# Kernel optimization log

Measured on AMD Instinct MI355X. Metric: run time of the kernel, lower is better.

The kernel has to match this reference:

```python
import jax, jax.numpy as jnp
import numpy as np

B, T, E, H = 4, 2048, 1024, 16
D = E // H

def setup_inputs() -> dict:
    key = jax.random.key(0)
    ks = jax.random.split(key, 8)
    s = 0.02
    return {
        "q": jax.random.normal(ks[0], (B, T, E), dtype=jnp.float32),
        "k": jax.random.normal(ks[1], (B, T, E), dtype=jnp.float32),
        "v": jax.random.normal(ks[2], (B, T, E), dtype=jnp.float32),
        "Wq": jax.random.normal(ks[3], (E, E), dtype=jnp.float32) * s,
        "Wk": jax.random.normal(ks[4], (E, E), dtype=jnp.float32) * s,
        "Wv": jax.random.normal(ks[5], (E, E), dtype=jnp.float32) * s,
        "Wp": jax.random.normal(ks[6], (E, E), dtype=jnp.float32) * s,
        "bp": jnp.zeros((E,), dtype=jnp.float32),
    }

def reference(q, k, v, Wq, Wk, Wv, Wp, bp):
    # Linear projections (torch Linear: x @ W.T). NOTE: original code computes
    # key from the already-projected query (k = self.key(q)); external k is unused.
    qp = q @ Wq.T                      # [B,T,E]
    kp = qp @ Wk.T                     # [B,T,E]  <- faithful quirk
    vp = v @ Wv.T                      # [B,T,E]
    qh = qp.reshape(B, T, H, D).transpose(0, 2, 1, 3)  # [B,H,T,D]
    kh = kp.reshape(B, T, H, D).transpose(0, 2, 1, 3)
    vh = vp.reshape(B, T, H, D).transpose(0, 2, 1, 3)
    # Faithful quirk: att = scores / D**(-1/2) == scores * sqrt(D)
    scale = jnp.float32(D) ** 0.5
    att = jnp.einsum('bhtd,bhsd->bhts', qh, kh) * scale  # [B,H,T,T]
    causal = jnp.tril(jnp.ones((T, T), dtype=bool))
    att = jnp.where(causal, att, -jnp.inf)
    att = jax.nn.softmax(att, axis=-1)
    y = jnp.einsum('bhts,bhsd->bhtd', att, vh)           # [B,H,T,D]
    y = y.transpose(0, 2, 1, 3).reshape(B, T, E)
    return y @ Wp.T + bp
```

## Files before the change

### kernel.cpp

```cpp
#include <hip/hip_runtime.h>


typedef unsigned short u16;
typedef unsigned int   u32;
typedef __attribute__((ext_vector_type(8))) __bf16 bf16x8;
typedef __attribute__((ext_vector_type(8))) u16    u16x8;
typedef __attribute__((ext_vector_type(4))) u16    u16x4;
typedef __attribute__((ext_vector_type(4))) float  f32x4;
typedef __attribute__((ext_vector_type(4))) int    i32x4;

#define DEV static __device__ __forceinline__

DEV u16 f2bf(float x){ union{float f;u32 u;}v; v.f=x; u32 r=v.u+0x7fffu+((v.u>>16)&1u); return (u16)(r>>16); }
DEV float bf2f(u16 b){ union{u32 u;float f;}v; v.u=((u32)b)<<16; return v.f; }
DEV f32x4 zero4(){ f32x4 z={0.f,0.f,0.f,0.f}; return z; }
DEV f32x4 mfma16(bf16x8 a, bf16x8 b, f32x4 c){ return __builtin_amdgcn_mfma_f32_16x16x32_bf16(a,b,c,0,0,0); }
DEV void gld16(const u16* g, u16* l){
  __builtin_amdgcn_global_load_lds((const __attribute__((address_space(1))) u32*)g,
                                   (__attribute__((address_space(3))) u32*)l, 16, 0, 0);
}

constexpr int B_=4, T_=2048, E_=1024;
constexpr int M_=B_*T_;

__global__ __launch_bounds__(256) void cvt_w(const float* __restrict__ Wq, const float* __restrict__ Wk,
                                             const float* __restrict__ Wv,
                                             u16* wqh,u16* wql,u16* wkh,u16* wkl,u16* wvb)
{
  const int j=blockIdx.y;
  const float* s = (j==0)?Wq : (j==1)?Wk : Wv;
  size_t i = ((size_t)blockIdx.x*256 + threadIdx.x)*4;
  f32x4 v = *reinterpret_cast<const f32x4*>(s+i);
  u16x4 h,l;
#pragma unroll
  for(int t=0;t<4;t++){ u16 hh=f2bf(v[t]); h[t]=hh; l[t]=f2bf(v[t]-bf2f(hh)); }
  if(j==0){ *reinterpret_cast<u16x4*>(wqh+i)=h; *reinterpret_cast<u16x4*>(wql+i)=l; }
  else if(j==1){ *reinterpret_cast<u16x4*>(wkh+i)=h; *reinterpret_cast<u16x4*>(wkl+i)=l; }
  else { *reinterpret_cast<u16x4*>(wvb+i)=h; }
}

__global__ __launch_bounds__(256) void cvt_a(const float* __restrict__ q, const float* __restrict__ v,
                                             u16* qsh,u16* qsl,u16* vb)
{
  const int j=blockIdx.y;
  size_t i = ((size_t)blockIdx.x*256 + threadIdx.x)*4;
  const float* s = (j==0)?q:v;
  f32x4 x = *reinterpret_cast<const f32x4*>(s+i);
  u16x4 h,l;
#pragma unroll
  for(int t=0;t<4;t++){ u16 hh=f2bf(x[t]); h[t]=hh; l[t]=f2bf(x[t]-bf2f(hh)); }
  if(j==0){ *reinterpret_cast<u16x4*>(qsh+i)=h; *reinterpret_cast<u16x4*>(qsl+i)=l; }
  else { *reinterpret_cast<u16x4*>(vb+i)=h; }
}

template<int ASPLIT,int WSPLIT,int WF32,int OMODE>
__global__ __launch_bounds__(256)
void gemm(const u16* __restrict__ Ah, const u16* __restrict__ Al,
          const u16* __restrict__ Wh, const u16* __restrict__ Wl,
          const float* __restrict__ Wf, const float* __restrict__ bias,
          u16* __restrict__ Ohi, u16* __restrict__ Olo, float* __restrict__ Of)
{
  constexpr int WPIT = WF32 ? 40 : 32;
  __shared__ u16 sAh[128*32];
  __shared__ u16 sAl[ASPLIT?128*32:8];
  __shared__ u16 sBh[128*WPIT];
  __shared__ u16 sBl[WSPLIT?128*WPIT:8];

  const int tid=threadIdx.x, wave=tid>>6, lane=tid&63;
  const int quad=lane>>4, l16=lane&15;
  const int wm=(wave>>1)*64, wn=(wave&1)*64;
  const int n0=blockIdx.x*128, m0=blockIdx.y*128;

  f32x4 acc[4][4];
#pragma unroll
  for(int i=0;i<4;i++)
#pragma unroll
    for(int j=0;j<4;j++) acc[i][j]=zero4();

  for(int k0=0;k0<E_;k0+=32){
#pragma unroll
    for(int it=0;it<2;it++){
      const int chunk=it*256+tid;
      const size_t goff=(size_t)(m0+(chunk>>2))*E_ + k0 + (chunk&3)*8;
      u16* ldst=&sAh[(it*256+wave*64)*8];
      gld16(Ah+goff, ldst);
      if(ASPLIT) gld16(Al+goff, &sAl[(it*256+wave*64)*8]);
    }
    if(!WF32){
#pragma unroll
      for(int it=0;it<2;it++){
        const int chunk=it*256+tid;
        const size_t goff=(size_t)(n0+(chunk>>2))*E_ + k0 + (chunk&3)*8;
        gld16(Wh+goff, &sBh[(it*256+wave*64)*8]);
        if(WSPLIT) gld16(Wl+goff, &sBl[(it*256+wave*64)*8]);
      }
    } else {
#pragma unroll
      for(int it=0;it<4;it++){
        int c=it*256+tid, row=c>>3, col=(c&7)*4;
        f32x4 w=*reinterpret_cast<const f32x4*>(Wf + (size_t)(n0+row)*E_ + k0+col);
        u16x4 h;
#pragma unroll
        for(int t=0;t<4;t++) h[t]=f2bf(w[t]);
        *reinterpret_cast<u16x4*>(&sBh[row*WPIT+col])=h;
      }
    }
    __syncthreads();

    bf16x8 ah[4],bh[4],al[4],bl[4];
#pragma unroll
    for(int i=0;i<4;i++){
      ah[i]=*reinterpret_cast<const bf16x8*>(&sAh[(wm+i*16+l16)*32+quad*8]);
      bh[i]=*reinterpret_cast<const bf16x8*>(&sBh[(wn+i*16+l16)*WPIT+quad*8]);
      if(ASPLIT) al[i]=*reinterpret_cast<const bf16x8*>(&sAl[(wm+i*16+l16)*32+quad*8]);
      if(WSPLIT) bl[i]=*reinterpret_cast<const bf16x8*>(&sBl[(wn+i*16+l16)*WPIT+quad*8]);
    }
#pragma unroll
    for(int i=0;i<4;i++)
#pragma unroll
      for(int j=0;j<4;j++){
        acc[i][j]=mfma16(ah[i],bh[j],acc[i][j]);
        if(WSPLIT) acc[i][j]=mfma16(ah[i],bl[j],acc[i][j]);
        if(ASPLIT) acc[i][j]=mfma16(al[i],bh[j],acc[i][j]);
      }
    __syncthreads();
  }

#pragma unroll
  for(int i=0;i<4;i++)
#pragma unroll
    for(int j=0;j<4;j++){
      const int col=n0+wn+j*16+l16;
#pragma unroll
      for(int r=0;r<4;r++){
        const int row=m0+wm+i*16+quad*4+r;
        const size_t idx=(size_t)row*E_+col;
        float v=acc[i][j][r];
        if(OMODE==2)      Of[idx]=v+bias[col];
        else if(OMODE==1) Ohi[idx]=f2bf(v);
        else { u16 hh=f2bf(v); Ohi[idx]=hh; Olo[idx]=f2bf(v-bf2f(hh)); }
      }
    }
}

__global__ __launch_bounds__(256)
void attn(const u16* __restrict__ qph, const u16* __restrict__ qpl,
          const u16* __restrict__ kph, const u16* __restrict__ kpl,
          const u16* __restrict__ vph, u16* __restrict__ yout)
{
  constexpr int VP=72;
  __shared__ u16 sKh[64*64];
  __shared__ u16 sKl[64*64];
  __shared__ u16 sV [64*VP];

  const int tid=threadIdx.x, wave=tid>>6, lane=tid&63;
  const int quad=lane>>4, l16=lane&15;
  const int qt = (int)(gridDim.x-1-blockIdx.x)>>6;
  const int bh = blockIdx.x&63;
  const int b=bh>>4, h=bh&15;
  const int qr0=qt*128+wave*32;

  bf16x8 qfh[2][2], qfl[2][2];
#pragma unroll
  for(int mt=0;mt<2;mt++)
#pragma unroll
    for(int ksv=0;ksv<2;ksv++){
      size_t off=(size_t)(b*T_+qr0+mt*16+l16)*E_ + h*64 + ksv*32 + quad*8;
      qfh[mt][ksv]=*reinterpret_cast<const bf16x8*>(qph+off);
      qfl[mt][ksv]=*reinterpret_cast<const bf16x8*>(qpl+off);
    }

  float mst[2]={-1e30f,-1e30f}, lst[2]={0.f,0.f};
  f32x4 oacc[2][4];
#pragma unroll
  for(int mt=0;mt<2;mt++)
#pragma unroll
    for(int dt=0;dt<4;dt++) oacc[mt][dt]=zero4();

  const int nkt=2*(qt+1);
  for(int kt=0;kt<nkt;kt++){
    const int s0=kt*64;
    __syncthreads();
#pragma unroll
    for(int it=0;it<2;it++){
      const int chunk=it*256+tid;
      const size_t off=(size_t)(b*T_+s0+(chunk>>3))*E_ + h*64 + (chunk&7)*8;
      gld16(kph+off, &sKh[(it*256+wave*64)*8]);
      gld16(kpl+off, &sKl[(it*256+wave*64)*8]);
    }
#pragma unroll
    for(int it=0;it<2;it++){
      const int c=it*256+tid, s=c&63, dc=(c>>6)*8;
      u16x8 vv=*reinterpret_cast<const u16x8*>(vph + (size_t)(b*T_+s0+s)*E_ + h*64 + dc);
#pragma unroll
      for(int j=0;j<8;j++) sV[(dc+j)*VP+s]=vv[j];
    }
    __syncthreads();

    if(s0<=qr0+31){
      f32x4 sacc[4][2];
#pragma unroll
      for(int st=0;st<4;st++)
#pragma unroll
        for(int mt=0;mt<2;mt++) sacc[st][mt]=zero4();
#pragma unroll
      for(int st=0;st<4;st++)
#pragma unroll
        for(int ksv=0;ksv<2;ksv++){
          bf16x8 kh=*reinterpret_cast<const bf16x8*>(&sKh[(st*16+l16)*64+ksv*32+quad*8]);
          bf16x8 kl=*reinterpret_cast<const bf16x8*>(&sKl[(st*16+l16)*64+ksv*32+quad*8]);
#pragma unroll
          for(int mt=0;mt<2;mt++){
            sacc[st][mt]=mfma16(kh,qfh[mt][ksv],sacc[st][mt]);
            sacc[st][mt]=mfma16(kl,qfh[mt][ksv],sacc[st][mt]);
            sacc[st][mt]=mfma16(kh,qfl[mt][ksv],sacc[st][mt]);
          }
        }
      const bool needmask=(s0+63>qr0);
      u32 pk_[4][2][2];
#pragma unroll
      for(int mt=0;mt<2;mt++){
        const int qrow=qr0+mt*16+l16;
        float mloc=-1e30f;
#pragma unroll
        for(int st=0;st<4;st++)
#pragma unroll
          for(int r=0;r<4;r++){
            float v=sacc[st][mt][r]*8.0f;
            if(needmask && (s0+st*16+quad*4+r>qrow)) v=-1e30f;
            sacc[st][mt][r]=v;
            mloc=fmaxf(mloc,v);
          }
        mloc=fmaxf(mloc,__shfl_xor(mloc,16,64));
        mloc=fmaxf(mloc,__shfl_xor(mloc,32,64));
        const float nm=fmaxf(mst[mt],mloc);
        const float alpha=__expf(mst[mt]-nm);
        mst[mt]=nm;
        float rs=0.f;
#pragma unroll
        for(int st=0;st<4;st++)
#pragma unroll
          for(int r=0;r<4;r++){
            float p=__expf(sacc[st][mt][r]-nm);
            sacc[st][mt][r]=p;
            rs+=p;
          }
        rs+=__shfl_xor(rs,16,64);
        rs+=__shfl_xor(rs,32,64);
        lst[mt]=lst[mt]*alpha+rs;
#pragma unroll
        for(int dt=0;dt<4;dt++) oacc[mt][dt]*=alpha;
#pragma unroll
        for(int st=0;st<4;st++){
          pk_[st][mt][0]=(u32)f2bf(sacc[st][mt][0]) | ((u32)f2bf(sacc[st][mt][1])<<16);
          pk_[st][mt][1]=(u32)f2bf(sacc[st][mt][2]) | ((u32)f2bf(sacc[st][mt][3])<<16);
        }
      }
      const int srcA=(2*(quad&1))*16+l16, srcB=srcA+16;
      const bool hs=(quad>=2);
#pragma unroll
      for(int ksv=0;ksv<2;ksv++){
        bf16x8 b2[2];
#pragma unroll
        for(int mt=0;mt<2;mt++){
          int e0=__shfl((int)pk_[2*ksv  ][mt][0],srcA,64);
          int g0=__shfl((int)pk_[2*ksv+1][mt][0],srcA,64);
          int e1=__shfl((int)pk_[2*ksv  ][mt][1],srcA,64);
          int g1=__shfl((int)pk_[2*ksv+1][mt][1],srcA,64);
          int e2=__shfl((int)pk_[2*ksv  ][mt][0],srcB,64);
          int g2=__shfl((int)pk_[2*ksv+1][mt][0],srcB,64);
          int e3=__shfl((int)pk_[2*ksv  ][mt][1],srcB,64);
          int g3=__shfl((int)pk_[2*ksv+1][mt][1],srcB,64);
          i32x4 bd={ hs?g0:e0, hs?g1:e1, hs?g2:e2, hs?g3:e3 };
          b2[mt]=*reinterpret_cast<bf16x8*>(&bd);
        }
#pragma unroll
        for(int dt=0;dt<4;dt++){
          bf16x8 va=*reinterpret_cast<const bf16x8*>(&sV[(dt*16+l16)*VP+ksv*32+quad*8]);
#pragma unroll
          for(int mt=0;mt<2;mt++)
            oacc[mt][dt]=mfma16(va,b2[mt],oacc[mt][dt]);
        }
      }
    }
  }
#pragma unroll
  for(int mt=0;mt<2;mt++){
    const float inv=1.0f/lst[mt];
    const size_t rb=(size_t)(b*T_+qr0+mt*16+l16)*E_ + h*64;
#pragma unroll
    for(int dt=0;dt<4;dt++){
      u16x4 o4;
#pragma unroll
      for(int r=0;r<4;r++) o4[r]=f2bf(oacc[mt][dt][r]*inv);
      *reinterpret_cast<u16x4*>(yout + rb + dt*16 + quad*4)=o4;
    }
  }
}

extern "C" void kernel_launch(void* const* d_in, const int* in_sizes, int n_in,
                              void* d_out, int out_size, void* d_ws, size_t ws_size,
                              hipStream_t stream)
{
  const float* q =(const float*)d_in[0];
  const float* v =(const float*)d_in[2];
  const float* Wq=(const float*)d_in[3];
  const float* Wk=(const float*)d_in[4];
  const float* Wv=(const float*)d_in[5];
  const float* Wp=(const float*)d_in[6];
  const float* bp=(const float*)d_in[7];
  float* out=(float*)d_out;

  const size_t NE=(size_t)M_*E_;
  u16* ws0=(u16*)d_ws;
  u16* ws1=ws0+NE;
  u16* ws2=ws1+NE;
  u16* ws3=ws2+NE;
  u16* ws4=ws3+NE;
  u16* ws5=ws4+NE;
  const size_t WE=(size_t)E_*E_;
  u16* wqh=(u16*)d_out;
  u16* wql=wqh+WE;
  u16* wkh=wql+WE;
  u16* wkl=wkh+WE;
  u16* wvb=wkl+WE;

  dim3 blk(256);
  cvt_a<<<dim3(NE/1024,2), blk, 0, stream>>>(q, v, ws2, ws3, ws5);
  cvt_w<<<dim3(WE/1024,3), blk, 0, stream>>>(Wq, Wk, Wv, wqh, wql, wkh, wkl, wvb);

  dim3 g(E_/128, M_/128);
  gemm<1,1,0,0><<<g, blk, 0, stream>>>(ws2, ws3, wqh, wql, nullptr, nullptr, ws0, ws1, nullptr);
  gemm<1,1,0,0><<<g, blk, 0, stream>>>(ws0, ws1, wkh, wkl, nullptr, nullptr, ws2, ws3, nullptr);
  gemm<0,0,0,1><<<g, blk, 0, stream>>>(ws5, nullptr, wvb, nullptr, nullptr, nullptr, ws4, nullptr, nullptr);
  attn<<<dim3(16*64), blk, 0, stream>>>(ws0, ws1, ws2, ws3, ws4, ws5);
  gemm<0,0,1,2><<<g, blk, 0, stream>>>(ws5, nullptr, nullptr, nullptr, Wp, bp, nullptr, nullptr, out);
}
```

Measured before the change: 484.7 us.

## Interleave hi/lo bf16 splits, swizzle LDS tiles, widen GEMM K-step, use exp2 softmax

```diff
diff --git a/kernel.cpp b/kernel.cpp
--- a/kernel.cpp
+++ b/kernel.cpp
@@ -19,57 +19,77 @@
   __builtin_amdgcn_global_load_lds((const __attribute__((address_space(1))) u32*)g,
                                    (__attribute__((address_space(3))) u32*)l, 16, 0, 0);
 }
+DEV u32 pkbf(float a, float b){
+  union{float f;u32 u;}x,y; x.f=a; y.f=b;
+  return __builtin_amdgcn_perm(y.u+0x8000u, x.u+0x8000u, 0x07060302u);
+}
 
 constexpr int B_=4, T_=2048, E_=1024;
 constexpr int M_=B_*T_;
-
-__global__ __launch_bounds__(256) void cvt_w(const float* __restrict__ Wq, const float* __restrict__ Wk,
-                                             const float* __restrict__ Wv,
-                                             u16* wqh,u16* wql,u16* wkh,u16* wkl,u16* wvb)
+constexpr float L2E8 = 11.5415603f;
+
+__global__ __launch_bounds__(256)
+void cvt_a(const float* __restrict__ q, const float* __restrict__ v,
+           u16* __restrict__ qi, u16* __restrict__ vb)
 {
   const int j=blockIdx.y;
-  const float* s = (j==0)?Wq : (j==1)?Wk : Wv;
-  size_t i = ((size_t)blockIdx.x*256 + threadIdx.x)*4;
-  f32x4 v = *reinterpret_cast<const f32x4*>(s+i);
-  u16x4 h,l;
-#pragma unroll
-  for(int t=0;t<4;t++){ u16 hh=f2bf(v[t]); h[t]=hh; l[t]=f2bf(v[t]-bf2f(hh)); }
-  if(j==0){ *reinterpret_cast<u16x4*>(wqh+i)=h; *reinterpret_cast<u16x4*>(wql+i)=l; }
-  else if(j==1){ *reinterpret_cast<u16x4*>(wkh+i)=h; *reinterpret_cast<u16x4*>(wkl+i)=l; }
-  else { *reinterpret_cast<u16x4*>(wvb+i)=h; }
-}
-
-__global__ __launch_bounds__(256) void cvt_a(const float* __restrict__ q, const float* __restrict__ v,
-                                             u16* qsh,u16* qsl,u16* vb)
+  const size_t e=((size_t)blockIdx.x*256+threadIdx.x)*8;
+  const float* s=(j==0)?q:v;
+  f32x4 x0=*reinterpret_cast<const f32x4*>(s+e);
+  f32x4 x1=*reinterpret_cast<const f32x4*>(s+e+4);
+  u16x8 h,l;
+#pragma unroll
+  for(int t=0;t<4;t++){
+    u16 hh=f2bf(x0[t]); h[t]=hh; l[t]=f2bf(x0[t]-bf2f(hh));
+    u16 h2=f2bf(x1[t]); h[t+4]=h2; l[t+4]=f2bf(x1[t]-bf2f(h2));
+  }
+  if(j==0){
+    const size_t row=e>>10, k=e&1023;
+    u16* d=qi + row*2048 + (k>>3)*16;
+    *reinterpret_cast<u16x8*>(d)=h;
+    *reinterpret_cast<u16x8*>(d+8)=l;
+  } else {
+    *reinterpret_cast<u16x8*>(vb+e)=h;
+  }
+}
+
+__global__ __launch_bounds__(256)
+void cvt_w(const float* __restrict__ Wq, const float* __restrict__ Wk, const float* __restrict__ Wv,
+           u16* __restrict__ wqi, u16* __restrict__ wki, u16* __restrict__ wvb)
 {
   const int j=blockIdx.y;
-  size_t i = ((size_t)blockIdx.x*256 + threadIdx.x)*4;
-  const float* s = (j==0)?q:v;
-  f32x4 x = *reinterpret_cast<const f32x4*>(s+i);
-  u16x4 h,l;
-#pragma unroll
-  for(int t=0;t<4;t++){ u16 hh=f2bf(x[t]); h[t]=hh; l[t]=f2bf(x[t]-bf2f(hh)); }
-  if(j==0){ *reinterpret_cast<u16x4*>(qsh+i)=h; *reinterpret_cast<u16x4*>(qsl+i)=l; }
-  else { *reinterpret_cast<u16x4*>(vb+i)=h; }
-}
-
-template<int ASPLIT,int WSPLIT,int WF32,int OMODE>
+  const size_t e=((size_t)blockIdx.x*256+threadIdx.x)*8;
+  const float* s=(j==0)?Wq:(j==1)?Wk:Wv;
+  f32x4 x0=*reinterpret_cast<const f32x4*>(s+e);
+  f32x4 x1=*reinterpret_cast<const f32x4*>(s+e+4);
+  u16x8 h,l;
+#pragma unroll
+  for(int t=0;t<4;t++){
+    u16 hh=f2bf(x0[t]); h[t]=hh; l[t]=f2bf(x0[t]-bf2f(hh));
+    u16 h2=f2bf(x1[t]); h[t+4]=h2; l[t+4]=f2bf(x1[t]-bf2f(h2));
+  }
+  if(j==2){ *reinterpret_cast<u16x8*>(wvb+e)=h; return; }
+  u16* base=(j==0)?wqi:wki;
+  const size_t row=e>>10, k=e&1023;
+  u16* d=base + row*2048 + (k>>3)*16;
+  *reinterpret_cast<u16x8*>(d)=h;
+  *reinterpret_cast<u16x8*>(d+8)=l;
+}
+
+template<int SPLIT,int WF32,int OMODE>
 __global__ __launch_bounds__(256)
-void gemm(const u16* __restrict__ Ah, const u16* __restrict__ Al,
-          const u16* __restrict__ Wh, const u16* __restrict__ Wl,
+void gemm(const u16* __restrict__ Ag, const u16* __restrict__ Bg,
           const float* __restrict__ Wf, const float* __restrict__ bias,
-          u16* __restrict__ Ohi, u16* __restrict__ Olo, float* __restrict__ Of)
-{
-  constexpr int WPIT = WF32 ? 40 : 32;
-  __shared__ u16 sAh[128*32];
-  __shared__ u16 sAl[ASPLIT?128*32:8];
-  __shared__ u16 sBh[128*WPIT];
-  __shared__ u16 sBl[WSPLIT?128*WPIT:8];
+          u16* __restrict__ Ob, float* __restrict__ Of)
+{
+  __shared__ u16 sA[128*64];
+  __shared__ u16 sB[WF32 ? 128*68 : 128*64];
 
   const int tid=threadIdx.x, wave=tid>>6, lane=tid&63;
-  const int quad=lane>>4, l16=lane&15;
+  const int quad=lane>>4, l16=lane&15, sw=l16&7;
   const int wm=(wave>>1)*64, wn=(wave&1)*64;
   const int n0=blockIdx.x*128, m0=blockIdx.y*128;
+  constexpr int KSTEP = SPLIT?32:64;
 
   f32x4 acc[4][4];
 #pragma unroll
@@ -77,52 +97,71 @@
 #pragma unroll
     for(int j=0;j<4;j++) acc[i][j]=zero4();
 
-  for(int k0=0;k0<E_;k0+=32){
-#pragma unroll
-    for(int it=0;it<2;it++){
-      const int chunk=it*256+tid;
-      const size_t goff=(size_t)(m0+(chunk>>2))*E_ + k0 + (chunk&3)*8;
-      u16* ldst=&sAh[(it*256+wave*64)*8];
-      gld16(Ah+goff, ldst);
-      if(ASPLIT) gld16(Al+goff, &sAl[(it*256+wave*64)*8]);
+  for(int k0=0;k0<E_;k0+=KSTEP){
+#pragma unroll
+    for(int it=0;it<4;it++){
+      const int c=it*256+tid, row=c>>3, j=(c&7)^(row&7);
+      const u16* ga = SPLIT ? Ag + (size_t)(m0+row)*2048 + (size_t)(k0>>3)*16 + j*8
+                            : Ag + (size_t)(m0+row)*1024 + k0 + j*8;
+      gld16(ga, &sA[(it*256+wave*64)*8]);
     }
     if(!WF32){
 #pragma unroll
-      for(int it=0;it<2;it++){
-        const int chunk=it*256+tid;
-        const size_t goff=(size_t)(n0+(chunk>>2))*E_ + k0 + (chunk&3)*8;
-        gld16(Wh+goff, &sBh[(it*256+wave*64)*8]);
-        if(WSPLIT) gld16(Wl+goff, &sBl[(it*256+wave*64)*8]);
+      for(int it=0;it<4;it++){
+        const int c=it*256+tid, row=c>>3, j=(c&7)^(row&7);
+        const u16* gb = SPLIT ? Bg + (size_t)(n0+row)*2048 + (size_t)(k0>>3)*16 + j*8
+                              : Bg + (size_t)(n0+row)*1024 + k0 + j*8;
+        gld16(gb, &sB[(it*256+wave*64)*8]);
       }
     } else {
 #pragma unroll
-      for(int it=0;it<4;it++){
-        int c=it*256+tid, row=c>>3, col=(c&7)*4;
-        f32x4 w=*reinterpret_cast<const f32x4*>(Wf + (size_t)(n0+row)*E_ + k0+col);
-        u16x4 h;
-#pragma unroll
-        for(int t=0;t<4;t++) h[t]=f2bf(w[t]);
-        *reinterpret_cast<u16x4*>(&sBh[row*WPIT+col])=h;
+      for(int it=0;it<8;it++){
+        const int idx=it*256+tid, row=idx>>4, col=(idx&15)*4;
+        f32x4 w=*reinterpret_cast<const f32x4*>(Wf + (size_t)(n0+row)*1024 + k0+col);
+        u16x4 hh;
+#pragma unroll
+        for(int t=0;t<4;t++) hh[t]=f2bf(w[t]);
+        *reinterpret_cast<u16x4*>(&sB[row*68+col])=hh;
       }
     }
     __syncthreads();
 
-    bf16x8 ah[4],bh[4],al[4],bl[4];
-#pragma unroll
-    for(int i=0;i<4;i++){
-      ah[i]=*reinterpret_cast<const bf16x8*>(&sAh[(wm+i*16+l16)*32+quad*8]);
-      bh[i]=*reinterpret_cast<const bf16x8*>(&sBh[(wn+i*16+l16)*WPIT+quad*8]);
-      if(ASPLIT) al[i]=*reinterpret_cast<const bf16x8*>(&sAl[(wm+i*16+l16)*32+quad*8]);
-      if(WSPLIT) bl[i]=*reinterpret_cast<const bf16x8*>(&sBl[(wn+i*16+l16)*WPIT+quad*8]);
-    }
-#pragma unroll
-    for(int i=0;i<4;i++)
-#pragma unroll
-      for(int j=0;j<4;j++){
-        acc[i][j]=mfma16(ah[i],bh[j],acc[i][j]);
-        if(WSPLIT) acc[i][j]=mfma16(ah[i],bl[j],acc[i][j]);
-        if(ASPLIT) acc[i][j]=mfma16(al[i],bh[j],acc[i][j]);
-      }
+    if(SPLIT){
+      bf16x8 ahh[4],ahl[4],bhh[4],bhl[4];
+#pragma unroll
+      for(int i=0;i<4;i++){
+        const u16* pa=&sA[(wm+i*16+l16)*64];
+        const u16* pb=&sB[(wn+i*16+l16)*64];
+        ahh[i]=*reinterpret_cast<const bf16x8*>(&pa[((2*quad  )^sw)*8]);
+        ahl[i]=*reinterpret_cast<const bf16x8*>(&pa[((2*quad+1)^sw)*8]);
+        bhh[i]=*reinterpret_cast<const bf16x8*>(&pb[((2*quad  )^sw)*8]);
+        bhl[i]=*reinterpret_cast<const bf16x8*>(&pb[((2*quad+1)^sw)*8]);
+      }
+#pragma unroll
+      for(int i=0;i<4;i++)
+#pragma unroll
+        for(int j=0;j<4;j++){
+          acc[i][j]=mfma16(ahh[i],bhh[j],acc[i][j]);
+          acc[i][j]=mfma16(ahh[i],bhl[j],acc[i][j]);
+          acc[i][j]=mfma16(ahl[i],bhh[j],acc[i][j]);
+        }
+    } else {
+#pragma unroll
+      for(int kk=0;kk<2;kk++){
+        bf16x8 a[4],b[4];
+#pragma unroll
+        for(int i=0;i<4;i++){
+          a[i]=*reinterpret_cast<const bf16x8*>(&sA[(wm+i*16+l16)*64 + (((kk*4+quad)^sw)*8)]);
+          b[i]= WF32 ? *reinterpret_cast<const bf16x8*>(&sB[(wn+i*16+l16)*68 + kk*32+quad*8])
+                     : *reinterpret_cast<const bf16x8*>(&sB[(wn+i*16+l16)*64 + (((kk*4+quad)^sw)*8)]);
+        }
+#pragma unroll
+        for(int i=0;i<4;i++)
+#pragma unroll
+          for(int j=0;j<4;j++)
+            acc[i][j]=mfma16(a[i],b[j],acc[i][j]);
+      }
+    }
     __syncthreads();
   }
 
@@ -134,29 +173,30 @@
 #pragma unroll
       for(int r=0;r<4;r++){
         const int row=m0+wm+i*16+quad*4+r;
-        const size_t idx=(size_t)row*E_+col;
         float v=acc[i][j][r];
-        if(OMODE==2)      Of[idx]=v+bias[col];
-        else if(OMODE==1) Ohi[idx]=f2bf(v);
-        else { u16 hh=f2bf(v); Ohi[idx]=hh; Olo[idx]=f2bf(v-bf2f(hh)); }
+        if(OMODE==2)      Of[(size_t)row*E_+col]=v+bias[col];
+        else if(OMODE==1) Ob[(size_t)row*E_+col]=f2bf(v);
+        else {
+          u16 hh=f2bf(v);
+          const size_t base=(size_t)row*2048 + (size_t)(col>>3)*16 + (col&7);
+          Ob[base]=hh; Ob[base+8]=f2bf(v-bf2f(hh));
+        }
       }
     }
 }
 
 __global__ __launch_bounds__(256)
-void attn(const u16* __restrict__ qph, const u16* __restrict__ qpl,
-          const u16* __restrict__ kph, const u16* __restrict__ kpl,
+void attn(const u16* __restrict__ qpi, const u16* __restrict__ kpi,
           const u16* __restrict__ vph, u16* __restrict__ yout)
 {
-  constexpr int VP=72;
-  __shared__ u16 sKh[64*64];
-  __shared__ u16 sKl[64*64];
-  __shared__ u16 sV [64*VP];
+  constexpr int VP=68;
+  __shared__ u16 sK[64*128];
+  __shared__ u16 sV[64*VP];
 
   const int tid=threadIdx.x, wave=tid>>6, lane=tid&63;
-  const int quad=lane>>4, l16=lane&15;
-  const int qt = (int)(gridDim.x-1-blockIdx.x)>>6;
-  const int bh = blockIdx.x&63;
+  const int quad=lane>>4, l16=lane&15, sw=l16&7;
+  const int qt=(int)(gridDim.x-1-blockIdx.x)>>6;
+  const int bh=blockIdx.x&63;
   const int b=bh>>4, h=bh&15;
   const int qr0=qt*128+wave*32;
 
@@ -165,9 +205,9 @@
   for(int mt=0;mt<2;mt++)
 #pragma unroll
     for(int ksv=0;ksv<2;ksv++){
-      size_t off=(size_t)(b*T_+qr0+mt*16+l16)*E_ + h*64 + ksv*32 + quad*8;
-      qfh[mt][ksv]=*reinterpret_cast<const bf16x8*>(qph+off);
-      qfl[mt][ksv]=*reinterpret_cast<const bf16x8*>(qpl+off);
+      const size_t off=(size_t)(b*T_+qr0+mt*16+l16)*2048 + h*128 + (ksv*4+quad)*16;
+      qfh[mt][ksv]=*reinterpret_cast<const bf16x8*>(qpi+off);
+      qfl[mt][ksv]=*reinterpret_cast<const bf16x8*>(qpi+off+8);
     }
 
   float mst[2]={-1e30f,-1e30f}, lst[2]={0.f,0.f};
@@ -182,16 +222,15 @@
     const int s0=kt*64;
     __syncthreads();
 #pragma unroll
-    for(int it=0;it<2;it++){
-      const int chunk=it*256+tid;
-      const size_t off=(size_t)(b*T_+s0+(chunk>>3))*E_ + h*64 + (chunk&7)*8;
-      gld16(kph+off, &sKh[(it*256+wave*64)*8]);
-      gld16(kpl+off, &sKl[(it*256+wave*64)*8]);
+    for(int it=0;it<4;it++){
+      const int c=it*256+tid, row=c>>4, j=(c&15)^(row&7);
+      gld16(kpi + (size_t)(b*T_+s0+row)*2048 + h*128 + j*8,
+            &sK[(it*256+wave*64)*8]);
     }
 #pragma unroll
     for(int it=0;it<2;it++){
       const int c=it*256+tid, s=c&63, dc=(c>>6)*8;
-      u16x8 vv=*reinterpret_cast<const u16x8*>(vph + (size_t)(b*T_+s0+s)*E_ + h*64 + dc);
+      u16x8 vv=*reinterpret_cast<const u16x8*>(vph + (size_t)(b*T_+s0+s)*1024 + h*64 + dc);
 #pragma unroll
       for(int j=0;j<8;j++) sV[(dc+j)*VP+s]=vv[j];
     }
@@ -207,8 +246,9 @@
       for(int st=0;st<4;st++)
 #pragma unroll
         for(int ksv=0;ksv<2;ksv++){
-          bf16x8 kh=*reinterpret_cast<const bf16x8*>(&sKh[(st*16+l16)*64+ksv*32+quad*8]);
-          bf16x8 kl=*reinterpret_cast<const bf16x8*>(&sKl[(st*16+l16)*64+ksv*32+quad*8]);
+          const u16* pk=&sK[(st*16+l16)*128];
+          bf16x8 kh=*reinterpret_cast<const bf16x8*>(&pk[((2*(ksv*4+quad)  )^sw)*8]);
+          bf16x8 kl=*reinterpret_cast<const bf16x8*>(&pk[((2*(ksv*4+quad)+1)^sw)*8]);
 #pragma unroll
           for(int mt=0;mt<2;mt++){
             sacc[st][mt]=mfma16(kh,qfh[mt][ksv],sacc[st][mt]);
@@ -226,7 +266,7 @@
         for(int st=0;st<4;st++)
 #pragma unroll
           for(int r=0;r<4;r++){
-            float v=sacc[st][mt][r]*8.0f;
+            float v=sacc[st][mt][r];
             if(needmask && (s0+st*16+quad*4+r>qrow)) v=-1e30f;
             sacc[st][mt][r]=v;
             mloc=fmaxf(mloc,v);
@@ -234,14 +274,15 @@
         mloc=fmaxf(mloc,__shfl_xor(mloc,16,64));
         mloc=fmaxf(mloc,__shfl_xor(mloc,32,64));
         const float nm=fmaxf(mst[mt],mloc);
-        const float alpha=__expf(mst[mt]-nm);
+        const float alpha=exp2f((mst[mt]-nm)*L2E8);
         mst[mt]=nm;
+        const float cexp=nm*L2E8;
         float rs=0.f;
 #pragma unroll
         for(int st=0;st<4;st++)
 #pragma unroll
           for(int r=0;r<4;r++){
-            float p=__expf(sacc[st][mt][r]-nm);
+            float p=exp2f(__builtin_fmaf(sacc[st][mt][r],L2E8,-cexp));
             sacc[st][mt][r]=p;
             rs+=p;
           }
@@ -252,8 +293,8 @@
         for(int dt=0;dt<4;dt++) oacc[mt][dt]*=alpha;
 #pragma unroll
         for(int st=0;st<4;st++){
-          pk_[st][mt][0]=(u32)f2bf(sacc[st][mt][0]) | ((u32)f2bf(sacc[st][mt][1])<<16);
-          pk_[st][mt][1]=(u32)f2bf(sacc[st][mt][2]) | ((u32)f2bf(sacc[st][mt][3])<<16);
+          pk_[st][mt][0]=pkbf(sacc[st][mt][0],sacc[st][mt][1]);
+          pk_[st][mt][1]=pkbf(sacc[st][mt][2],sacc[st][mt][3]);
         }
       }
       const int srcA=(2*(quad&1))*16+l16, srcB=srcA+16;
@@ -287,7 +328,7 @@
 #pragma unroll
   for(int mt=0;mt<2;mt++){
     const float inv=1.0f/lst[mt];
-    const size_t rb=(size_t)(b*T_+qr0+mt*16+l16)*E_ + h*64;
+    const size_t rb=(size_t)(b*T_+qr0+mt*16+l16)*1024 + h*64;
 #pragma unroll
     for(int dt=0;dt<4;dt++){
       u16x4 o4;
@@ -312,27 +353,27 @@
   float* out=(float*)d_out;
 
   const size_t NE=(size_t)M_*E_;
-  u16* ws0=(u16*)d_ws;
-  u16* ws1=ws0+NE;
-  u16* ws2=ws1+NE;
-  u16* ws3=ws2+NE;
-  u16* ws4=ws3+NE;
-  u16* ws5=ws4+NE;
   const size_t WE=(size_t)E_*E_;
-  u16* wqh=(u16*)d_out;
-  u16* wql=wqh+WE;
-  u16* wkh=wql+WE;
-  u16* wkl=wkh+WE;
-  u16* wvb=wkl+WE;
+  u16* wsv=(u16*)d_ws;
+  u16* qsl_i=wsv;
+  u16* qp_i =wsv+2*NE;
+  u16* kp_i =wsv;
+  u16* vpb  =wsv+4*NE;
+  u16* ybf  =wsv+5*NE;
+  u16* og   =(u16*)d_out;
+  u16* wq_i =og;
+  u16* wk_i =og+2*WE;
+  u16* wv_b =og+4*WE;
+  u16* vb   =og+5*WE;
 
   dim3 blk(256);
-  cvt_a<<<dim3(NE/1024,2), blk, 0, stream>>>(q, v, ws2, ws3, ws5);
-  cvt_w<<<dim3(WE/1024,3), blk, 0, stream>>>(Wq, Wk, Wv, wqh, wql, wkh, wkl, wvb);
+  cvt_a<<<dim3(NE/2048,2), blk, 0, stream>>>(q, v, qsl_i, vb);
+  cvt_w<<<dim3(WE/2048,3), blk, 0, stream>>>(Wq, Wk, Wv, wq_i, wk_i, wv_b);
 
   dim3 g(E_/128, M_/128);
-  gemm<1,1,0,0><<<g, blk, 0, stream>>>(ws2, ws3, wqh, wql, nullptr, nullptr, ws0, ws1, nullptr);
-  gemm<1,1,0,0><<<g, blk, 0, stream>>>(ws0, ws1, wkh, wkl, nullptr, nullptr, ws2, ws3, nullptr);
-  gemm<0,0,0,1><<<g, blk, 0, stream>>>(ws5, nullptr, wvb, nullptr, nullptr, nullptr, ws4, nullptr, nullptr);
-  attn<<<dim3(16*64), blk, 0, stream>>>(ws0, ws1, ws2, ws3, ws4, ws5);
-  gemm<0,0,1,2><<<g, blk, 0, stream>>>(ws5, nullptr, nullptr, nullptr, Wp, bp, nullptr, nullptr, out);
-}
+  gemm<1,0,0><<<g, blk, 0, stream>>>(qsl_i, wq_i, nullptr, nullptr, qp_i, nullptr);
+  gemm<1,0,0><<<g, blk, 0, stream>>>(qp_i,  wk_i, nullptr, nullptr, kp_i, nullptr);
+  gemm<0,0,1><<<g, blk, 0, stream>>>(vb,    wv_b, nullptr, nullptr, vpb,  nullptr);
+  attn<<<dim3(1024), blk, 0, stream>>>(qp_i, kp_i, vpb, ybf);
+  gemm<0,1,2><<<g, blk, 0, stream>>>(ybf, nullptr, Wp, bp, nullptr, out);
+}
```

Measured after the change: 459.9 us. -5.1%, faster.
